# Kernel optimization log

Hardware: AMD Instinct MI355X
Metric: run time of the kernel (lower is better)

## Reference

```python
import jax, jax.numpy as jnp
import numpy as np

DX = 8e-6      # pixel pitch (m)
Z = 0.05       # propagation distance (m)
B, C, H, W = 8, 3, 1024, 1024


def setup_inputs() -> dict:
    key = jax.random.key(0)
    k1, k2 = jax.random.split(key)
    x_real = jax.random.normal(k1, (B, C, H, W), dtype=jnp.float32)
    x_imag = jax.random.normal(k2, (B, C, H, W), dtype=jnp.float32)
    wavelengths = jnp.asarray([450e-9, 532e-9, 632.8e-9], dtype=jnp.float32)
    return {"x_real": x_real, "x_imag": x_imag, "wavelengths": wavelengths}


def _transfer_function(wavelengths, h, w, dx, z):
    # Angular-spectrum transfer function per wavelength: [C, H, W] complex64
    fx = jnp.fft.fftfreq(w, d=dx).astype(jnp.float32)  # [W]
    fy = jnp.fft.fftfreq(h, d=dx).astype(jnp.float32)  # [H]
    f2 = fy[:, None] ** 2 + fx[None, :] ** 2           # [H, W]
    lam = wavelengths[:, None, None]                   # [C, 1, 1]
    arg = 1.0 - (lam ** 2) * f2[None]                  # [C, H, W]
    kz = (2.0 * jnp.pi / lam) * z * jnp.sqrt(jnp.maximum(arg, 0.0))
    Hc = jnp.exp(1j * kz.astype(jnp.complex64))
    # zero out evanescent components
    return jnp.where(arg > 0.0, Hc, jnp.zeros((), dtype=jnp.complex64))


def reference(x_real, x_imag, wavelengths):
    # Batched angular-spectrum propagation, one wavelength per channel.
    x = (x_real + 1j * x_imag).astype(jnp.complex64)   # [B, C, H, W]
    Hc = _transfer_function(wavelengths, H, W, DX, Z)  # [C, H, W]
    Xf = jnp.fft.fft2(x, axes=(-2, -1))
    out = jnp.fft.ifft2(Xf * Hc[None], axes=(-2, -1))  # [B, C, H, W] complex
    # return real/imag stacked so output is a float tensor: [2, B, C, H, W]
    return jnp.stack([out.real.astype(jnp.float32), out.imag.astype(jnp.float32)], axis=0)
```

## Files before the change

### kernel.cpp

```cpp
#include <hip/hip_runtime.h>
#include <math.h>


#define NIMG 24

__device__ __forceinline__ float2 cadd(float2 a, float2 b){ return make_float2(a.x+b.x, a.y+b.y); }
__device__ __forceinline__ float2 csub(float2 a, float2 b){ return make_float2(a.x-b.x, a.y-b.y); }
__device__ __forceinline__ float2 cmul(float2 a, float c, float s){ return make_float2(a.x*c - a.y*s, a.x*s + a.y*c); }

__device__ __forceinline__ int SW(int j) {
    int b = j << 3;
    return b ^ (((b >> 7) & 7) << 4);
}

__device__ __forceinline__ float2 computeH(float lam, int ky, int kx) {
    int iy = (ky < 512) ? ky : ky - 1024;
    int ix = (kx < 512) ? kx : kx - 1024;
    const double recip = 1.0 / (1024.0 * 8e-06);
    float fy = (float)((double)iy * recip);
    float fx = (float)((double)ix * recip);
    float f2  = __fadd_rn(__fmul_rn(fy, fy), __fmul_rn(fx, fx));
    float l2  = __fmul_rn(lam, lam);
    float arg = __fsub_rn(1.0f, __fmul_rn(l2, f2));
    float2 h = make_float2(0.0f, 0.0f);
    if (arg > 0.0f) {
        float t  = __fdiv_rn(6.28318530717958647692f, lam);
        t        = __fmul_rn(t, 0.05f);
        float kz = __fmul_rn(t, __fsqrt_rn(arg));
        double s, c;
        sincos((double)kz, &s, &c);
        const float sc = 9.5367431640625e-07f;
        h = make_float2((float)c * sc, (float)s * sc);
    }
    return h;
}

__global__ __launch_bounds__(256) void build_H_T(float2* __restrict__ Htab,
                                                 const float* __restrict__ wl) {
    int idx = blockIdx.x * 256 + threadIdx.x;
    int c   = idx >> 20;
    int rem = idx & 1048575;
    Htab[idx] = computeH(wl[c], rem & 1023, rem >> 10);
}

template<int SIGN>
__device__ __forceinline__ void dft4nt(float2& a0, float2& a1, float2& a2, float2& a3) {
    float2 t0 = cadd(a0, a2), t1 = csub(a0, a2);
    float2 t2 = cadd(a1, a3), t3 = csub(a1, a3);
    a0 = cadd(t0, t2);
    a2 = csub(t0, t2);
    a1 = make_float2(t1.x - SIGN * t3.y, t1.y + SIGN * t3.x);
    a3 = make_float2(t1.x + SIGN * t3.y, t1.y - SIGN * t3.x);
}
template<int SIGN>
__device__ __forceinline__ void dft4(float2& a0, float2& a1, float2& a2, float2& a3,
                                     float c1, float s1) {
    float c2 = c1*c1 - s1*s1, s2 = 2.f*c1*s1;
    float c3 = c2*c1 - s2*s1, s3 = s2*c1 + c2*s1;
    a1 = cmul(a1, c1, s1);
    a2 = cmul(a2, c2, s2);
    a3 = cmul(a3, c3, s3);
    dft4nt<SIGN>(a0, a1, a2, a3);
}

#define WSYNC() do { asm volatile("s_waitcnt lgkmcnt(0)" ::: "memory"); \
                     __builtin_amdgcn_wave_barrier(); } while (0)

template<int SIGN>
__device__ __forceinline__ void wave_fft(char* cb, int l) {
    const float SPI8   = SIGN * 0.39269908169872415481f;
    const float SPI32  = SIGN * 0.09817477042468103870f;
    const float SPI128 = SIGN * 0.02454369260617025967f;
    const float SPI512 = SIGN * 0.00613592315154256492f;
    const int swzE = (((l >> 4)    ) & 7) << 4;
    const int swzO = (((l >> 4) + 4) & 7) << 4;
    char* rbE = cb + ((8 * l) ^ swzE);
    char* rbO = cb + ((8 * l) ^ swzO);
    float2 v[4][4];

    #pragma unroll
    for (int k = 0; k < 4; ++k) {
        #pragma unroll
        for (int r = 0; r < 4; ++r) {
            const int tt = k + 4 * r;
            v[k][r] = *(const float2*)(((tt & 1) ? rbO : rbE) + 512 * tt);
        }
    }
    #pragma unroll
    for (int k = 0; k < 4; ++k) dft4nt<SIGN>(v[k][0], v[k][1], v[k][2], v[k][3]);
    dft4nt<SIGN>(v[0][0], v[1][0], v[2][0], v[3][0]);
    #pragma unroll
    for (int q = 1; q < 4; ++q) {
        float s1, c1; __sincosf((float)q * SPI8, &s1, &c1);
        dft4<SIGN>(v[0][q], v[1][q], v[2][q], v[3][q], c1, s1);
    }
    {
        char* wb = cb + 128 * l;
        const int L7 = l & 7;
        #pragma unroll
        for (int p = 0; p < 4; ++p) {
            *(float4*)(wb + 16 * ((2*p+0) ^ L7)) =
                make_float4(v[p][0].x, v[p][0].y, v[p][1].x, v[p][1].y);
            *(float4*)(wb + 16 * ((2*p+1) ^ L7)) =
                make_float4(v[p][2].x, v[p][2].y, v[p][3].x, v[p][3].y);
        }
    }
    WSYNC();

    #pragma unroll
    for (int k = 0; k < 4; ++k) {
        #pragma unroll
        for (int r = 0; r < 4; ++r) {
            const int tt = k + 4 * r;
            v[k][r] = *(const float2*)(((tt & 1) ? rbO : rbE) + 512 * tt);
        }
    }
    {
        const int jm2 = l & 15;
        float s1, c1; __sincosf((float)jm2 * SPI32, &s1, &c1);
        #pragma unroll
        for (int k = 0; k < 4; ++k) dft4<SIGN>(v[k][0], v[k][1], v[k][2], v[k][3], c1, s1);
        const int lo8 = 8 * (l & 15);
        const int hi  = 2048 * (l >> 4);
        #pragma unroll
        for (int q = 0; q < 4; ++q) {
            float s1b, c1b; __sincosf((float)(jm2 + 16 * q) * SPI128, &s1b, &c1b);
            dft4<SIGN>(v[0][q], v[1][q], v[2][q], v[3][q], c1b, s1b);
            #pragma unroll
            for (int p = 0; p < 4; ++p) {
                const int K = ((q + 4 * p) & 7) << 4;
                *(float2*)(cb + (lo8 ^ K) + hi + 128 * q + 512 * p) = v[p][q];
            }
        }
    }
    WSYNC();

    #pragma unroll
    for (int m = 0; m < 4; ++m) {
        #pragma unroll
        for (int r = 0; r < 4; ++r) {
            const int tt = m + 4 * r;
            v[m][r] = *(const float2*)(((tt & 1) ? rbO : rbE) + 512 * tt);
        }
    }
    #pragma unroll
    for (int m = 0; m < 4; ++m) {
        float s1, c1; __sincosf((float)(l + 64 * m) * SPI512, &s1, &c1);
        dft4<SIGN>(v[m][0], v[m][1], v[m][2], v[m][3], c1, s1);
        #pragma unroll
        for (int q = 0; q < 4; ++q) {
            const int tt = m + 4 * q;
            *(float2*)(((tt & 1) ? rbO : rbE) + 512 * tt) = v[m][q];
        }
    }
}

__global__ __launch_bounds__(512, 4) void k1_rows_T(const float* __restrict__ xr,
                                                    const float* __restrict__ xi,
                                                    float2* __restrict__ T) {
    __shared__ float4 ldsb[4096];
    char* lds = (char*)ldsb;
    const int t = threadIdx.x, w = t >> 6, l = t & 63;
    const int img = blockIdx.x >> 7;
    const int y0  = (blockIdx.x & 127) << 3;
    const long long ib = (long long)img << 20;
    char* cb = lds + 8192 * w;

    {
        const float4* rr = (const float4*)(xr + ib + (long long)(y0 + w) * 1024);
        const float4* ri = (const float4*)(xi + ib + (long long)(y0 + w) * 1024);
        const int swz = ((l >> 2) & 7) << 4;
        #pragma unroll
        for (int k = 0; k < 4; ++k) {
            float4 a = rr[64 * k + l], b = ri[64 * k + l];
            *(float4*)(cb + 2048 * k + ((32 * l) ^ swz))      = make_float4(a.x, b.x, a.y, b.y);
            *(float4*)(cb + 2048 * k + ((32 * l + 16) ^ swz)) = make_float4(a.z, b.z, a.w, b.w);
        }
    }
    WSYNC();
    wave_fft<-1>(cb, l);
    __syncthreads();

    {
        const int seg = t & 3;
        const int xb  = t >> 2;
        #pragma unroll
        for (int k = 0; k < 8; ++k) {
            int x = xb + 128 * k;
            float2 v0 = *(const float2*)(lds + 8192 * (2 * seg)     + SW(x));
            float2 v1 = *(const float2*)(lds + 8192 * (2 * seg + 1) + SW(x));
            *(float4*)(T + ib + (long long)x * 1024 + y0 + 2 * seg) =
                make_float4(v0.x, v0.y, v1.x, v1.y);
        }
    }
}

__global__ __launch_bounds__(256, 4) void k2_cols_H(float2* __restrict__ T,
                                                    const float2* __restrict__ Htab,
                                                    const float* __restrict__ wl) {
    __shared__ float4 ldsb[2048];
    char* lds = (char*)ldsb;
    const int t = threadIdx.x, w = t >> 6, l = t & 63;
    const int img = blockIdx.x >> 8;
    const int x   = ((blockIdx.x & 255) << 2) + w;
    const int lamIdx = img % 3;
    char* cb = lds + 8192 * w;
    float2* row = T + ((long long)img << 20) + (long long)x * 1024;
    const int swz = ((l >> 3) & 7) << 4;

    #pragma unroll
    for (int k = 0; k < 8; ++k) {
        float4 g = ((const float4*)row)[64 * k + l];
        *(float4*)(cb + 1024 * k + ((16 * l) ^ swz)) = g;
    }
    WSYNC();
    wave_fft<-1>(cb, l);
    WSYNC();
    {
        const float2* hrow = Htab ? (Htab + ((long long)lamIdx << 20) + (long long)x * 1024)
                                  : nullptr;
        const float lam = Htab ? 0.0f : wl[lamIdx];
        #pragma unroll
        for (int k = 0; k < 8; ++k) {
            float4* p = (float4*)(cb + 1024 * k + ((16 * l) ^ swz));
            float4 a = *p;
            float4 h;
            if (hrow) {
                h = ((const float4*)hrow)[64 * k + l];
            } else {
                int m = 128 * k + 2 * l;
                float2 h0 = computeH(lam, m,     x);
                float2 h1 = computeH(lam, m + 1, x);
                h = make_float4(h0.x, h0.y, h1.x, h1.y);
            }
            *p = make_float4(a.x * h.x - a.y * h.y, a.x * h.y + a.y * h.x,
                             a.z * h.z - a.w * h.w, a.z * h.w + a.w * h.z);
        }
    }
    WSYNC();
    wave_fft<1>(cb, l);
    WSYNC();
    #pragma unroll
    for (int k = 0; k < 8; ++k) {
        float4 g = *(const float4*)(cb + 1024 * k + ((16 * l) ^ swz));
        ((float4*)row)[64 * k + l] = g;
    }
}

__global__ __launch_bounds__(1024, 1) void k3_irows_T16(const float2* __restrict__ T,
                                                        float* __restrict__ outr,
                                                        float* __restrict__ outi) {
    extern __shared__ char lds[];
    const int t = threadIdx.x;
    const int img = blockIdx.x >> 6;
    const int y0  = (blockIdx.x & 63) << 4;
    const long long ib = (long long)img << 20;

    {
        const float4* src = (const float4*)(T + ib + (long long)t * 1024 + y0);
        const int sx = SW(t);
        #pragma unroll
        for (int p = 0; p < 8; ++p) {
            float4 g = src[p];
            *(float2*)(lds + 8192 * (2 * p)     + sx) = make_float2(g.x, g.y);
            *(float2*)(lds + 8192 * (2 * p + 1) + sx) = make_float2(g.z, g.w);
        }
    }
    __syncthreads();

    const int w = t >> 6, l = t & 63;
    char* cb = lds + 8192 * w;
    wave_fft<1>(cb, l);
    WSYNC();

    {
        float4* pr = (float4*)(outr + ib + (long long)(y0 + w) * 1024);
        float4* pi = (float4*)(outi + ib + (long long)(y0 + w) * 1024);
        const int swz = ((l >> 2) & 7) << 4;
        #pragma unroll
        for (int k = 0; k < 4; ++k) {
            float4 c0 = *(const float4*)(cb + 2048 * k + ((32 * l) ^ swz));
            float4 c1 = *(const float4*)(cb + 2048 * k + ((32 * l + 16) ^ swz));
            pr[64 * k + l] = make_float4(c0.x, c0.z, c1.x, c1.z);
            pi[64 * k + l] = make_float4(c0.y, c0.w, c1.y, c1.w);
        }
    }
}

extern "C" void kernel_launch(void* const* d_in, const int* in_sizes, int n_in,
                              void* d_out, int out_size, void* d_ws, size_t ws_size,
                              hipStream_t stream) {
    const float* xr = (const float*)d_in[0];
    const float* xi = (const float*)d_in[1];
    const float* wl = (const float*)d_in[2];
    float* out = (float*)d_out;

    const size_t planeElems = (size_t)NIMG * 1024 * 1024;
    float2* wsC = (float2*)d_ws;
    const size_t needC = planeElems * sizeof(float2);
    const size_t needH = (size_t)3 * 1024 * 1024 * sizeof(float2);
    float2* Htab = nullptr;
    if (ws_size >= needC + needH) {
        Htab = (float2*)((char*)d_ws + needC);
        build_H_T<<<12288, 256, 0, stream>>>(Htab, wl);
    }
    k1_rows_T<<<NIMG * 128, 512, 0, stream>>>(xr, xi, wsC);
    k2_cols_H<<<NIMG * 256, 256, 0, stream>>>(wsC, Htab, wl);
    k3_irows_T16<<<NIMG * 64, 1024, 131072, stream>>>(wsC, out, out + planeElems);
}
```

Baseline: 311.7 us.

## Load FFT inputs straight into registers and skip LDS staging round-trips

Splits the wave FFT into stages so the first stage reads directly from global memory into registers and the last stage keeps results in registers. The column kernel applies the transfer function in registers and writes to global without extra LDS passes. The row kernel moves to 16-row blocks of 1024 threads so its transposed writes are wider. This removes LDS staging loads and stores and barriers. The cost is narrower per-lane global accesses (float2 and scalar instead of float4) and higher register pressure.

```diff
diff --git a/kernel.cpp b/kernel.cpp
--- a/kernel.cpp
+++ b/kernel.cpp
@@ -66,18 +66,67 @@
 #define WSYNC() do { asm volatile("s_waitcnt lgkmcnt(0)" ::: "memory"); \
                      __builtin_amdgcn_wave_barrier(); } while (0)
 
-template<int SIGN>
-__device__ __forceinline__ void wave_fft(char* cb, int l) {
-    const float SPI8   = SIGN * 0.39269908169872415481f;
+
+__device__ __forceinline__ void ldsToRegs(char* cb, int l, float2 (&v)[4][4]) {
+    const int swzE = (((l >> 4)    ) & 7) << 4;
+    const int swzO = (((l >> 4) + 4) & 7) << 4;
+    char* rbE = cb + ((8 * l) ^ swzE);
+    char* rbO = cb + ((8 * l) ^ swzO);
+    #pragma unroll
+    for (int k = 0; k < 4; ++k) {
+        #pragma unroll
+        for (int r = 0; r < 4; ++r) {
+            const int tt = k + 4 * r;
+            v[k][r] = *(const float2*)(((tt & 1) ? rbO : rbE) + 512 * tt);
+        }
+    }
+}
+__device__ __forceinline__ void regsToLds(char* cb, int l, const float2 (&v)[4][4]) {
+    const int swzE = (((l >> 4)    ) & 7) << 4;
+    const int swzO = (((l >> 4) + 4) & 7) << 4;
+    char* rbE = cb + ((8 * l) ^ swzE);
+    char* rbO = cb + ((8 * l) ^ swzO);
+    #pragma unroll
+    for (int m = 0; m < 4; ++m) {
+        #pragma unroll
+        for (int q = 0; q < 4; ++q) {
+            const int tt = m + 4 * q;
+            *(float2*)(((tt & 1) ? rbO : rbE) + 512 * tt) = v[m][q];
+        }
+    }
+}
+
+template<int SIGN>
+__device__ __forceinline__ void fftA(char* cb, int l, float2 (&v)[4][4]) {
+    const float SPI8 = SIGN * 0.39269908169872415481f;
+    #pragma unroll
+    for (int k = 0; k < 4; ++k) dft4nt<SIGN>(v[k][0], v[k][1], v[k][2], v[k][3]);
+    dft4nt<SIGN>(v[0][0], v[1][0], v[2][0], v[3][0]);
+    #pragma unroll
+    for (int q = 1; q < 4; ++q) {
+        float s1, c1; __sincosf((float)q * SPI8, &s1, &c1);
+        dft4<SIGN>(v[0][q], v[1][q], v[2][q], v[3][q], c1, s1);
+    }
+    char* wb = cb + 128 * l;
+    const int L7 = l & 7;
+    #pragma unroll
+    for (int p = 0; p < 4; ++p) {
+        *(float4*)(wb + 16 * ((2*p+0) ^ L7)) =
+            make_float4(v[p][0].x, v[p][0].y, v[p][1].x, v[p][1].y);
+        *(float4*)(wb + 16 * ((2*p+1) ^ L7)) =
+            make_float4(v[p][2].x, v[p][2].y, v[p][3].x, v[p][3].y);
+    }
+}
+
+template<int SIGN>
+__device__ __forceinline__ void fftB(char* cb, int l) {
     const float SPI32  = SIGN * 0.09817477042468103870f;
     const float SPI128 = SIGN * 0.02454369260617025967f;
-    const float SPI512 = SIGN * 0.00613592315154256492f;
     const int swzE = (((l >> 4)    ) & 7) << 4;
     const int swzO = (((l >> 4) + 4) & 7) << 4;
     char* rbE = cb + ((8 * l) ^ swzE);
     char* rbO = cb + ((8 * l) ^ swzO);
     float2 v[4][4];
-
     #pragma unroll
     for (int k = 0; k < 4; ++k) {
         #pragma unroll
@@ -86,111 +135,71 @@
             v[k][r] = *(const float2*)(((tt & 1) ? rbO : rbE) + 512 * tt);
         }
     }
-    #pragma unroll
-    for (int k = 0; k < 4; ++k) dft4nt<SIGN>(v[k][0], v[k][1], v[k][2], v[k][3]);
-    dft4nt<SIGN>(v[0][0], v[1][0], v[2][0], v[3][0]);
-    #pragma unroll
-    for (int q = 1; q < 4; ++q) {
-        float s1, c1; __sincosf((float)q * SPI8, &s1, &c1);
-        dft4<SIGN>(v[0][q], v[1][q], v[2][q], v[3][q], c1, s1);
-    }
-    {
-        char* wb = cb + 128 * l;
-        const int L7 = l & 7;
+    const int jm2 = l & 15;
+    float s1, c1; __sincosf((float)jm2 * SPI32, &s1, &c1);
+    #pragma unroll
+    for (int k = 0; k < 4; ++k) dft4<SIGN>(v[k][0], v[k][1], v[k][2], v[k][3], c1, s1);
+    const int lo8 = 8 * (l & 15);
+    const int hi  = 2048 * (l >> 4);
+    #pragma unroll
+    for (int q = 0; q < 4; ++q) {
+        float s1b, c1b; __sincosf((float)(jm2 + 16 * q) * SPI128, &s1b, &c1b);
+        dft4<SIGN>(v[0][q], v[1][q], v[2][q], v[3][q], c1b, s1b);
         #pragma unroll
         for (int p = 0; p < 4; ++p) {
-            *(float4*)(wb + 16 * ((2*p+0) ^ L7)) =
-                make_float4(v[p][0].x, v[p][0].y, v[p][1].x, v[p][1].y);
-            *(float4*)(wb + 16 * ((2*p+1) ^ L7)) =
-                make_float4(v[p][2].x, v[p][2].y, v[p][3].x, v[p][3].y);
-        }
-    }
-    WSYNC();
-
-    #pragma unroll
-    for (int k = 0; k < 4; ++k) {
-        #pragma unroll
-        for (int r = 0; r < 4; ++r) {
-            const int tt = k + 4 * r;
-            v[k][r] = *(const float2*)(((tt & 1) ? rbO : rbE) + 512 * tt);
-        }
-    }
-    {
-        const int jm2 = l & 15;
-        float s1, c1; __sincosf((float)jm2 * SPI32, &s1, &c1);
-        #pragma unroll
-        for (int k = 0; k < 4; ++k) dft4<SIGN>(v[k][0], v[k][1], v[k][2], v[k][3], c1, s1);
-        const int lo8 = 8 * (l & 15);
-        const int hi  = 2048 * (l >> 4);
-        #pragma unroll
-        for (int q = 0; q < 4; ++q) {
-            float s1b, c1b; __sincosf((float)(jm2 + 16 * q) * SPI128, &s1b, &c1b);
-            dft4<SIGN>(v[0][q], v[1][q], v[2][q], v[3][q], c1b, s1b);
-            #pragma unroll
-            for (int p = 0; p < 4; ++p) {
-                const int K = ((q + 4 * p) & 7) << 4;
-                *(float2*)(cb + (lo8 ^ K) + hi + 128 * q + 512 * p) = v[p][q];
-            }
-        }
-    }
-    WSYNC();
-
-    #pragma unroll
-    for (int m = 0; m < 4; ++m) {
-        #pragma unroll
-        for (int r = 0; r < 4; ++r) {
-            const int tt = m + 4 * r;
-            v[m][r] = *(const float2*)(((tt & 1) ? rbO : rbE) + 512 * tt);
-        }
-    }
+            const int K = ((q + 4 * p) & 7) << 4;
+            *(float2*)(cb + (lo8 ^ K) + hi + 128 * q + 512 * p) = v[p][q];
+        }
+    }
+}
+
+template<int SIGN>
+__device__ __forceinline__ void fftC(int l, float2 (&v)[4][4]) {
+    const float SPI512 = SIGN * 0.00613592315154256492f;
     #pragma unroll
     for (int m = 0; m < 4; ++m) {
         float s1, c1; __sincosf((float)(l + 64 * m) * SPI512, &s1, &c1);
         dft4<SIGN>(v[m][0], v[m][1], v[m][2], v[m][3], c1, s1);
-        #pragma unroll
-        for (int q = 0; q < 4; ++q) {
-            const int tt = m + 4 * q;
-            *(float2*)(((tt & 1) ? rbO : rbE) + 512 * tt) = v[m][q];
-        }
-    }
-}
-
-__global__ __launch_bounds__(512, 4) void k1_rows_T(const float* __restrict__ xr,
+    }
+}
+
+__global__ __launch_bounds__(1024) void k1_rows_T16(const float* __restrict__ xr,
                                                     const float* __restrict__ xi,
                                                     float2* __restrict__ T) {
-    __shared__ float4 ldsb[4096];
-    char* lds = (char*)ldsb;
+    extern __shared__ char lds[];
     const int t = threadIdx.x, w = t >> 6, l = t & 63;
-    const int img = blockIdx.x >> 7;
-    const int y0  = (blockIdx.x & 127) << 3;
+    const int img = blockIdx.x >> 6;
+    const int y0  = (blockIdx.x & 63) << 4;
     const long long ib = (long long)img << 20;
     char* cb = lds + 8192 * w;
 
+    const float* rr = xr + ib + (long long)(y0 + w) * 1024;
+    const float* ri = xi + ib + (long long)(y0 + w) * 1024;
+    float2 v[4][4];
+    #pragma unroll
+    for (int k = 0; k < 4; ++k) {
+        #pragma unroll
+        for (int r = 0; r < 4; ++r) {
+            const int p = l + 64 * (k + 4 * r);
+            v[k][r] = make_float2(rr[p], ri[p]);
+        }
+    }
+    fftA<-1>(cb, l, v); WSYNC();
+    fftB<-1>(cb, l);    WSYNC();
+    ldsToRegs(cb, l, v);
+    fftC<-1>(l, v);
+    WSYNC();
+    regsToLds(cb, l, v);
+    __syncthreads();
+
     {
-        const float4* rr = (const float4*)(xr + ib + (long long)(y0 + w) * 1024);
-        const float4* ri = (const float4*)(xi + ib + (long long)(y0 + w) * 1024);
-        const int swz = ((l >> 2) & 7) << 4;
-        #pragma unroll
-        for (int k = 0; k < 4; ++k) {
-            float4 a = rr[64 * k + l], b = ri[64 * k + l];
-            *(float4*)(cb + 2048 * k + ((32 * l) ^ swz))      = make_float4(a.x, b.x, a.y, b.y);
-            *(float4*)(cb + 2048 * k + ((32 * l + 16) ^ swz)) = make_float4(a.z, b.z, a.w, b.w);
-        }
-    }
-    WSYNC();
-    wave_fft<-1>(cb, l);
-    __syncthreads();
-
-    {
-        const int seg = t & 3;
-        const int xb  = t >> 2;
-        #pragma unroll
-        for (int k = 0; k < 8; ++k) {
-            int x = xb + 128 * k;
-            float2 v0 = *(const float2*)(lds + 8192 * (2 * seg)     + SW(x));
-            float2 v1 = *(const float2*)(lds + 8192 * (2 * seg + 1) + SW(x));
-            *(float4*)(T + ib + (long long)x * 1024 + y0 + 2 * seg) =
-                make_float4(v0.x, v0.y, v1.x, v1.y);
+        float4* dst = (float4*)(T + ib + (long long)t * 1024 + y0);
+        const int sx = SW(t);
+        #pragma unroll
+        for (int p = 0; p < 8; ++p) {
+            float2 a = *(const float2*)(lds + 8192 * (2 * p)     + sx);
+            float2 b = *(const float2*)(lds + 8192 * (2 * p + 1) + sx);
+            dst[p] = make_float4(a.x, a.y, b.x, b.y);
         }
     }
 }
@@ -205,53 +214,68 @@
     const int x   = ((blockIdx.x & 255) << 2) + w;
     const int lamIdx = img % 3;
     char* cb = lds + 8192 * w;
-    float2* row = T + ((long long)img << 20) + (long long)x * 1024;
-    const int swz = ((l >> 3) & 7) << 4;
-
-    #pragma unroll
-    for (int k = 0; k < 8; ++k) {
-        float4 g = ((const float4*)row)[64 * k + l];
-        *(float4*)(cb + 1024 * k + ((16 * l) ^ swz)) = g;
+    float2* col = T + ((long long)img << 20) + (long long)x * 1024;
+
+    float2 v[4][4];
+    #pragma unroll
+    for (int k = 0; k < 4; ++k) {
+        #pragma unroll
+        for (int r = 0; r < 4; ++r)
+            v[k][r] = col[l + 64 * (k + 4 * r)];
+    }
+    fftA<-1>(cb, l, v); WSYNC();
+    fftB<-1>(cb, l);    WSYNC();
+
+    float2 h[4][4];
+    if (Htab) {
+        const float2* hrow = Htab + ((long long)lamIdx << 20) + (long long)x * 1024;
+        #pragma unroll
+        for (int m = 0; m < 4; ++m) {
+            #pragma unroll
+            for (int q = 0; q < 4; ++q)
+                h[m][q] = hrow[l + 64 * (m + 4 * q)];
+        }
+    } else {
+        const float lam = wl[lamIdx];
+        #pragma unroll
+        for (int m = 0; m < 4; ++m) {
+            #pragma unroll
+            for (int q = 0; q < 4; ++q)
+                h[m][q] = computeH(lam, l + 64 * (m + 4 * q), x);
+        }
+    }
+
+    ldsToRegs(cb, l, v);
+    fftC<-1>(l, v);
+
+    #pragma unroll
+    for (int m = 0; m < 4; ++m) {
+        #pragma unroll
+        for (int q = 0; q < 4; ++q) {
+            float2 a = v[m][q], hh = h[m][q];
+            v[m][q] = make_float2(a.x * hh.x - a.y * hh.y, a.x * hh.y + a.y * hh.x);
+        }
     }
     WSYNC();
-    wave_fft<-1>(cb, l);
-    WSYNC();
-    {
-        const float2* hrow = Htab ? (Htab + ((long long)lamIdx << 20) + (long long)x * 1024)
-                                  : nullptr;
-        const float lam = Htab ? 0.0f : wl[lamIdx];
-        #pragma unroll
-        for (int k = 0; k < 8; ++k) {
-            float4* p = (float4*)(cb + 1024 * k + ((16 * l) ^ swz));
-            float4 a = *p;
-            float4 h;
-            if (hrow) {
-                h = ((const float4*)hrow)[64 * k + l];
-            } else {
-                int m = 128 * k + 2 * l;
-                float2 h0 = computeH(lam, m,     x);
-                float2 h1 = computeH(lam, m + 1, x);
-                h = make_float4(h0.x, h0.y, h1.x, h1.y);
-            }
-            *p = make_float4(a.x * h.x - a.y * h.y, a.x * h.y + a.y * h.x,
-                             a.z * h.z - a.w * h.w, a.z * h.w + a.w * h.z);
-        }
-    }
-    WSYNC();
-    wave_fft<1>(cb, l);
-    WSYNC();
-    #pragma unroll
-    for (int k = 0; k < 8; ++k) {
-        float4 g = *(const float4*)(cb + 1024 * k + ((16 * l) ^ swz));
-        ((float4*)row)[64 * k + l] = g;
-    }
-}
-
-__global__ __launch_bounds__(1024, 1) void k3_irows_T16(const float2* __restrict__ T,
-                                                        float* __restrict__ outr,
-                                                        float* __restrict__ outi) {
+
+    fftA<1>(cb, l, v); WSYNC();
+    fftB<1>(cb, l);    WSYNC();
+    ldsToRegs(cb, l, v);
+    fftC<1>(l, v);
+
+    #pragma unroll
+    for (int m = 0; m < 4; ++m) {
+        #pragma unroll
+        for (int q = 0; q < 4; ++q)
+            col[l + 64 * (m + 4 * q)] = v[m][q];
+    }
+}
+
+__global__ __launch_bounds__(1024) void k3_irows_T16(const float2* __restrict__ T,
+                                                     float* __restrict__ outr,
+                                                     float* __restrict__ outi) {
     extern __shared__ char lds[];
-    const int t = threadIdx.x;
+    const int t = threadIdx.x, w = t >> 6, l = t & 63;
     const int img = blockIdx.x >> 6;
     const int y0  = (blockIdx.x & 63) << 4;
     const long long ib = (long long)img << 20;
@@ -268,21 +292,23 @@
     }
     __syncthreads();
 
-    const int w = t >> 6, l = t & 63;
     char* cb = lds + 8192 * w;
-    wave_fft<1>(cb, l);
-    WSYNC();
-
-    {
-        float4* pr = (float4*)(outr + ib + (long long)(y0 + w) * 1024);
-        float4* pi = (float4*)(outi + ib + (long long)(y0 + w) * 1024);
-        const int swz = ((l >> 2) & 7) << 4;
-        #pragma unroll
-        for (int k = 0; k < 4; ++k) {
-            float4 c0 = *(const float4*)(cb + 2048 * k + ((32 * l) ^ swz));
-            float4 c1 = *(const float4*)(cb + 2048 * k + ((32 * l + 16) ^ swz));
-            pr[64 * k + l] = make_float4(c0.x, c0.z, c1.x, c1.z);
-            pi[64 * k + l] = make_float4(c0.y, c0.w, c1.y, c1.w);
+    float2 v[4][4];
+    ldsToRegs(cb, l, v);
+    fftA<1>(cb, l, v); WSYNC();
+    fftB<1>(cb, l);    WSYNC();
+    ldsToRegs(cb, l, v);
+    fftC<1>(l, v);
+
+    float* pr = outr + ib + (long long)(y0 + w) * 1024;
+    float* pi = outi + ib + (long long)(y0 + w) * 1024;
+    #pragma unroll
+    for (int m = 0; m < 4; ++m) {
+        #pragma unroll
+        for (int q = 0; q < 4; ++q) {
+            const int p = l + 64 * (m + 4 * q);
+            pr[p] = v[m][q].x;
+            pi[p] = v[m][q].y;
         }
     }
 }
@@ -304,7 +330,7 @@
         Htab = (float2*)((char*)d_ws + needC);
         build_H_T<<<12288, 256, 0, stream>>>(Htab, wl);
     }
-    k1_rows_T<<<NIMG * 128, 512, 0, stream>>>(xr, xi, wsC);
+    k1_rows_T16<<<NIMG * 64, 1024, 131072, stream>>>(xr, xi, wsC);
     k2_cols_H<<<NIMG * 256, 256, 0, stream>>>(wsC, Htab, wl);
     k3_irows_T16<<<NIMG * 64, 1024, 131072, stream>>>(wsC, out, out + planeElems);
 }
```

Result: slower. 322.6 us (+3.5%).
